# Optimization experiments

Measured on AMD Instinct MI355X. Metric: run time of the kernel, lower is better.

## Reference

```python
import jax, jax.numpy as jnp
import numpy as np

N = 1_000_000
_I = np.arange(12)[:, None]
IDX1 = (2 * _I + np.array([-1, 0, 1])) % 24        # [12,3] neighbor gather for net1
IDX2 = (2 * _I + np.array([0, 1, 2])) % 24         # [12,3] for net2
IDX3 = (2 * _I + np.array([0, 1, 2, 3])) % 24      # [12,4] for net3
IDX_U1 = np.array([i for i in range(36) if i % 3 != 2])  # 24 columns kept
IDX_A = np.arange(-1, 33, 3) % 36                  # u[:, -1::3] style gather (12,)
IDX_B = np.arange(2, 36, 3)                        # (12,)


def _mlp(x, w0, b0, w1, b1, w2, b2):
    h = jax.nn.relu(x @ w0.T + b0)
    h = jax.nn.relu(h @ w1.T + b1)
    return h @ w2.T + b2


def setup_inputs() -> dict:
    key = jax.random.key(0)
    ks = jax.random.split(key, 24)
    d = {
        "t": 0,
        "u": jax.random.normal(ks[0], (N, 36), dtype=jnp.float32),
        "reg": jax.random.normal(ks[1], (37,), dtype=jnp.float32),
    }
    shapes = {
        "n1_w0": (3, 3), "n1_b0": (3,), "n1_w1": (6, 3), "n1_b1": (6,), "n1_w2": (3, 6), "n1_b2": (3,),
        "n2_w0": (3, 3), "n2_b0": (3,), "n2_w1": (6, 3), "n2_b1": (6,), "n2_w2": (3, 6), "n2_b2": (3,),
        "n3_w0": (4, 4), "n3_b0": (4,), "n3_w1": (6, 4), "n3_b1": (6,), "n3_w2": (2, 6), "n3_b2": (2,),
    }
    for i, (name, shp) in enumerate(shapes.items()):
        d[name] = jax.random.normal(ks[2 + i], shp, dtype=jnp.float32) * 0.3
    return d


def reference(t, u, reg,
              n1_w0, n1_b0, n1_w1, n1_b1, n1_w2, n1_b2,
              n2_w0, n2_b0, n2_w1, n2_b1, n2_w2, n2_b2,
              n3_w0, n3_b0, n3_w1, n3_b1, n3_w2, n3_b2):
    outreg = u * reg[1:] + reg[0]                 # [N,36]
    u1 = u[:, IDX_U1]                              # [N,24]
    x1 = u1[:, IDX1]                               # [N,12,3]
    x2 = u1[:, IDX2]                               # [N,12,3]
    x3 = u1[:, IDX3]                               # [N,12,4]
    o1 = _mlp(x1, n1_w0, n1_b0, n1_w1, n1_b1, n1_w2, n1_b2)  # [N,12,3]
    o2 = _mlp(x2, n2_w0, n2_b0, n2_w1, n2_b1, n2_w2, n2_b2)  # [N,12,3]
    o3 = _mlp(x3, n3_w0, n3_b0, n3_w1, n3_b1, n3_w2, n3_b2)  # [N,12,2]
    ua = u[:, IDX_A]                               # [N,12]
    ub = u[:, IDX_B]                               # [N,12]
    c0 = outreg[:, ::3] + o1[..., 0] + o1[..., 1] * ua + o1[..., 2] * ub
    c1 = outreg[:, 1::3] + o2[..., 0] + o2[..., 1] * ua + o2[..., 2] * ub
    c2 = outreg[:, 2::3] + o3[..., 0] + o3[..., 1] * ub
    # interleave back into strided slices ::3, 1::3, 2::3
    return jnp.stack([c0, c1, c2], axis=-1).reshape(u.shape[0], 36)
```

## Files before the change

### kernel.cpp

```cpp
#include <hip/hip_runtime.h>


typedef float f2 __attribute__((ext_vector_type(2)));

__device__ __forceinline__ f2 splat2(float x) { f2 v; v.x = x; v.y = x; return v; }
__device__ __forceinline__ f2 mk2(float a, float b) { f2 v; v.x = a; v.y = b; return v; }
__device__ __forceinline__ f2 fma2(f2 a, f2 b, f2 c) { return __builtin_elementwise_fma(a, b, c); }
__device__ __forceinline__ f2 relu2(f2 a) { return __builtin_elementwise_max(a, splat2(0.0f)); }

__device__ __forceinline__ void mlp_a2(f2 x0, f2 x1, f2 x2,
                                       const float* __restrict__ w0, const float* __restrict__ b0,
                                       const float* __restrict__ w1, const float* __restrict__ b1,
                                       const float* __restrict__ w2, const float* __restrict__ b2,
                                       f2& o0, f2& o1, f2& o2)
{
    f2 h0[3];
#pragma unroll
    for (int q = 0; q < 3; ++q) {
        f2 a = fma2(x0, splat2(w0[q*3+0]), splat2(b0[q]));
        a = fma2(x1, splat2(w0[q*3+1]), a);
        a = fma2(x2, splat2(w0[q*3+2]), a);
        h0[q] = relu2(a);
    }
    f2 h1[6];
#pragma unroll
    for (int q = 0; q < 6; ++q) {
        f2 a = fma2(h0[0], splat2(w1[q*3+0]), splat2(b1[q]));
        a = fma2(h0[1], splat2(w1[q*3+1]), a);
        a = fma2(h0[2], splat2(w1[q*3+2]), a);
        h1[q] = relu2(a);
    }
    f2 t[3];
#pragma unroll
    for (int q = 0; q < 3; ++q) {
        f2 a = fma2(h1[0], splat2(w2[q*6+0]), splat2(b2[q]));
#pragma unroll
        for (int i = 1; i < 6; ++i) a = fma2(h1[i], splat2(w2[q*6+i]), a);
        t[q] = a;
    }
    o0 = t[0]; o1 = t[1]; o2 = t[2];
}

__device__ __forceinline__ void mlp_b2(f2 x0, f2 x1, f2 x2, f2 x3,
                                       const float* __restrict__ w0, const float* __restrict__ b0,
                                       const float* __restrict__ w1, const float* __restrict__ b1,
                                       const float* __restrict__ w2, const float* __restrict__ b2,
                                       f2& o0, f2& o1)
{
    f2 h0[4];
#pragma unroll
    for (int q = 0; q < 4; ++q) {
        f2 a = fma2(x0, splat2(w0[q*4+0]), splat2(b0[q]));
        a = fma2(x1, splat2(w0[q*4+1]), a);
        a = fma2(x2, splat2(w0[q*4+2]), a);
        a = fma2(x3, splat2(w0[q*4+3]), a);
        h0[q] = relu2(a);
    }
    f2 h1[6];
#pragma unroll
    for (int q = 0; q < 6; ++q) {
        f2 a = fma2(h0[0], splat2(w1[q*4+0]), splat2(b1[q]));
        a = fma2(h0[1], splat2(w1[q*4+1]), a);
        a = fma2(h0[2], splat2(w1[q*4+2]), a);
        a = fma2(h0[3], splat2(w1[q*4+3]), a);
        h1[q] = relu2(a);
    }
    f2 t[2];
#pragma unroll
    for (int q = 0; q < 2; ++q) {
        f2 a = fma2(h1[0], splat2(w2[q*6+0]), splat2(b2[q]));
#pragma unroll
        for (int i = 1; i < 6; ++i) a = fma2(h1[i], splat2(w2[q*6+i]), a);
        t[q] = a;
    }
    o0 = t[0]; o1 = t[1];
}

#define ROWS_PB 64
#define TPB 192

__global__ __launch_bounds__(TPB) void mixmodel_kernel(
    const float* __restrict__ u, const float* __restrict__ reg,
    const float* __restrict__ w10, const float* __restrict__ b10,
    const float* __restrict__ w11, const float* __restrict__ b11,
    const float* __restrict__ w12, const float* __restrict__ b12,
    const float* __restrict__ w20, const float* __restrict__ b20,
    const float* __restrict__ w21, const float* __restrict__ b21,
    const float* __restrict__ w22, const float* __restrict__ b22,
    const float* __restrict__ w30, const float* __restrict__ b30,
    const float* __restrict__ w31, const float* __restrict__ b31,
    const float* __restrict__ w32, const float* __restrict__ b32,
    float* __restrict__ out, int n)
{
    __shared__ float4 s4[ROWS_PB * 9];
    __shared__ float  sreg[37];

    const int brow = blockIdx.x * ROWS_PB;

    {
        const float4* __restrict__ g = reinterpret_cast<const float4*>(u + (size_t)brow * 36);
        const int wid  = threadIdx.x >> 6;
        const int lane = threadIdx.x & 63;
#pragma unroll
        for (int w = 0; w < 3; ++w) {
            const int base = w * TPB + wid * 64;
            __builtin_amdgcn_global_load_lds(
                (const __attribute__((address_space(1))) void*)(g + base + lane),
                (__attribute__((address_space(3))) void*)(s4 + base),
                16, 0, 0);
        }
    }
    if (threadIdx.x < 37) sreg[threadIdx.x] = reg[threadIdx.x];
    asm volatile("s_waitcnt vmcnt(0)" ::: "memory");
    __syncthreads();

    const int rl = threadIdx.x / 3;
    const int r  = threadIdx.x - 3 * rl;
    const int row = brow + rl;
    if (row >= n) return;

    float w_[20];
#pragma unroll
    for (int t = 0; t < 5; ++t) {
        int idx = 3 * r + 8 + t;
        if (idx >= 9) idx -= 9;
        if (idx >= 9) idx -= 9;
        const float4 v = s4[rl * 9 + idx];
        w_[4*t+0] = v.x; w_[4*t+1] = v.y; w_[4*t+2] = v.z; w_[4*t+3] = v.w;
    }
#define W(k) w_[(k) + 4]

    const f2 r02 = splat2(sreg[0]);
    const float* rb = sreg + 12 * r;

    f2 c0[2], c1[2], c2[2];

#pragma unroll
    for (int P = 0; P < 2; ++P) {
        const int q = 6 * P;
        f2 a0, a1, a2;
        mlp_a2(mk2(W(q - 2), W(q + 1)), mk2(W(q), W(q + 3)), mk2(W(q + 1), W(q + 4)),
               w10, b10, w11, b11, w12, b12, a0, a1, a2);
        const f2 ua = mk2(W(q - 1), W(q + 2));
        const f2 ub = mk2(W(q + 2), W(q + 5));
        const f2 rv = mk2(rb[q + 1], rb[q + 4]);
        const f2 uv = mk2(W(q), W(q + 3));
        c0[P] = fma2(uv, rv, r02) + fma2(a2, ub, fma2(a1, ua, a0));
    }
#pragma unroll
    for (int P = 0; P < 2; ++P) {
        const int q = 6 * P;
        f2 a0, a1, a2;
        mlp_a2(mk2(W(q), W(q + 3)), mk2(W(q + 1), W(q + 4)), mk2(W(q + 3), W(q + 6)),
               w20, b20, w21, b21, w22, b22, a0, a1, a2);
        const f2 ua = mk2(W(q - 1), W(q + 2));
        const f2 ub = mk2(W(q + 2), W(q + 5));
        const f2 rv = mk2(rb[q + 2], rb[q + 5]);
        const f2 uv = mk2(W(q + 1), W(q + 4));
        c1[P] = fma2(uv, rv, r02) + fma2(a2, ub, fma2(a1, ua, a0));
    }
#pragma unroll
    for (int P = 0; P < 2; ++P) {
        const int q = 6 * P;
        f2 d0, d1;
        mlp_b2(mk2(W(q), W(q + 3)), mk2(W(q + 1), W(q + 4)),
               mk2(W(q + 3), W(q + 6)), mk2(W(q + 4), W(q + 7)),
               w30, b30, w31, b31, w32, b32, d0, d1);
        const f2 ub = mk2(W(q + 2), W(q + 5));
        const f2 rv = mk2(rb[q + 3], rb[q + 6]);
        c2[P] = fma2(ub, rv, r02) + fma2(d1, ub, d0);
    }
#undef W

    float4* __restrict__ o4 = reinterpret_cast<float4*>(out + (size_t)row * 36 + 12 * r);
    o4[0] = make_float4(c0[0].x, c1[0].x, c2[0].x, c0[0].y);
    o4[1] = make_float4(c1[0].y, c2[0].y, c0[1].x, c1[1].x);
    o4[2] = make_float4(c2[1].x, c0[1].y, c1[1].y, c2[1].y);
}

extern "C" void kernel_launch(void* const* d_in, const int* in_sizes, int n_in,
                              void* d_out, int out_size, void* d_ws, size_t ws_size,
                              hipStream_t stream)
{
    const float* u   = (const float*)d_in[1];
    const float* reg = (const float*)d_in[2];
    const float* w10 = (const float*)d_in[3];
    const float* b10 = (const float*)d_in[4];
    const float* w11 = (const float*)d_in[5];
    const float* b11 = (const float*)d_in[6];
    const float* w12 = (const float*)d_in[7];
    const float* b12 = (const float*)d_in[8];
    const float* w20 = (const float*)d_in[9];
    const float* b20 = (const float*)d_in[10];
    const float* w21 = (const float*)d_in[11];
    const float* b21 = (const float*)d_in[12];
    const float* w22 = (const float*)d_in[13];
    const float* b22 = (const float*)d_in[14];
    const float* w30 = (const float*)d_in[15];
    const float* b30 = (const float*)d_in[16];
    const float* w31 = (const float*)d_in[17];
    const float* b31 = (const float*)d_in[18];
    const float* w32 = (const float*)d_in[19];
    const float* b32 = (const float*)d_in[20];
    float* out = (float*)d_out;

    const int n = in_sizes[1] / 36;
    const int grid = (n + ROWS_PB - 1) / ROWS_PB;

    hipLaunchKernelGGL(mixmodel_kernel, dim3(grid), dim3(TPB), 0, stream,
                       u, reg, w10, b10, w11, b11, w12, b12,
                       w20, b20, w21, b21, w22, b22,
                       w30, b30, w31, b31, w32, b32, out, n);
}
```

Measured before the change: 71.05 us.

## Remap threads to row pairs with f2 packing across rows and nontemporal stores

```diff
diff --git a/kernel.cpp b/kernel.cpp
--- a/kernel.cpp
+++ b/kernel.cpp
@@ -114,68 +114,61 @@
     asm volatile("s_waitcnt vmcnt(0)" ::: "memory");
     __syncthreads();
 
-    const int rl = threadIdx.x / 3;
-    const int r  = threadIdx.x - 3 * rl;
-    const int row = brow + rl;
-    if (row >= n) return;
-
-    float w_[20];
-#pragma unroll
-    for (int t = 0; t < 5; ++t) {
-        int idx = 3 * r + 8 + t;
-        if (idx >= 9) idx -= 9;
-        if (idx >= 9) idx -= 9;
-        const float4 v = s4[rl * 9 + idx];
-        w_[4*t+0] = v.x; w_[4*t+1] = v.y; w_[4*t+2] = v.z; w_[4*t+3] = v.w;
-    }
-#define W(k) w_[(k) + 4]
+    const int t  = threadIdx.x;
+    const int rp = t / 6;
+    const int s  = t - 6 * rp;
+
+    const float* sf = reinterpret_cast<const float*>(s4);
+    const int va  = rp * 72 + 6 * s;
+    const int vaP = va - 2 + (s == 0 ? 36 : 0);
+    const int vaT = va + (s == 5 ? -36 : 0);
+
+    f2 P[10];
+#pragma unroll
+    for (int k = 0; k < 2; ++k) { P[k].x = sf[vaP + k];     P[k].y = sf[vaP + k + 36]; }
+#pragma unroll
+    for (int k = 0; k < 6; ++k) { P[k + 2].x = sf[va + k];  P[k + 2].y = sf[va + k + 36]; }
+#pragma unroll
+    for (int k = 6; k < 8; ++k) { P[k + 2].x = sf[vaT + k]; P[k + 2].y = sf[vaT + k + 36]; }
 
     const f2 r02 = splat2(sreg[0]);
-    const float* rb = sreg + 12 * r;
-
-    f2 c0[2], c1[2], c2[2];
-
-#pragma unroll
-    for (int P = 0; P < 2; ++P) {
-        const int q = 6 * P;
+    const float* rb = sreg + 6 * s;
+
+    f2 c_[6];
+
+#pragma unroll
+    for (int J = 0; J < 2; ++J) {
+        const int b = 3 * J;
         f2 a0, a1, a2;
-        mlp_a2(mk2(W(q - 2), W(q + 1)), mk2(W(q), W(q + 3)), mk2(W(q + 1), W(q + 4)),
-               w10, b10, w11, b11, w12, b12, a0, a1, a2);
-        const f2 ua = mk2(W(q - 1), W(q + 2));
-        const f2 ub = mk2(W(q + 2), W(q + 5));
-        const f2 rv = mk2(rb[q + 1], rb[q + 4]);
-        const f2 uv = mk2(W(q), W(q + 3));
-        c0[P] = fma2(uv, rv, r02) + fma2(a2, ub, fma2(a1, ua, a0));
-    }
-#pragma unroll
-    for (int P = 0; P < 2; ++P) {
-        const int q = 6 * P;
+        mlp_a2(P[b], P[b + 2], P[b + 3], w10, b10, w11, b11, w12, b12, a0, a1, a2);
+        c_[3*J + 0] = fma2(P[b + 2], splat2(rb[b + 1]), r02)
+                    + fma2(a2, P[b + 4], fma2(a1, P[b + 1], a0));
+    }
+#pragma unroll
+    for (int J = 0; J < 2; ++J) {
+        const int b = 3 * J;
         f2 a0, a1, a2;
-        mlp_a2(mk2(W(q), W(q + 3)), mk2(W(q + 1), W(q + 4)), mk2(W(q + 3), W(q + 6)),
-               w20, b20, w21, b21, w22, b22, a0, a1, a2);
-        const f2 ua = mk2(W(q - 1), W(q + 2));
-        const f2 ub = mk2(W(q + 2), W(q + 5));
-        const f2 rv = mk2(rb[q + 2], rb[q + 5]);
-        const f2 uv = mk2(W(q + 1), W(q + 4));
-        c1[P] = fma2(uv, rv, r02) + fma2(a2, ub, fma2(a1, ua, a0));
-    }
-#pragma unroll
-    for (int P = 0; P < 2; ++P) {
-        const int q = 6 * P;
+        mlp_a2(P[b + 2], P[b + 3], P[b + 5], w20, b20, w21, b21, w22, b22, a0, a1, a2);
+        c_[3*J + 1] = fma2(P[b + 3], splat2(rb[b + 2]), r02)
+                    + fma2(a2, P[b + 4], fma2(a1, P[b + 1], a0));
+    }
+#pragma unroll
+    for (int J = 0; J < 2; ++J) {
+        const int b = 3 * J;
         f2 d0, d1;
-        mlp_b2(mk2(W(q), W(q + 3)), mk2(W(q + 1), W(q + 4)),
-               mk2(W(q + 3), W(q + 6)), mk2(W(q + 4), W(q + 7)),
-               w30, b30, w31, b31, w32, b32, d0, d1);
-        const f2 ub = mk2(W(q + 2), W(q + 5));
-        const f2 rv = mk2(rb[q + 3], rb[q + 6]);
-        c2[P] = fma2(ub, rv, r02) + fma2(d1, ub, d0);
-    }
-#undef W
-
-    float4* __restrict__ o4 = reinterpret_cast<float4*>(out + (size_t)row * 36 + 12 * r);
-    o4[0] = make_float4(c0[0].x, c1[0].x, c2[0].x, c0[0].y);
-    o4[1] = make_float4(c1[0].y, c2[0].y, c0[1].x, c1[1].x);
-    o4[2] = make_float4(c2[1].x, c0[1].y, c1[1].y, c2[1].y);
+        mlp_b2(P[b + 2], P[b + 3], P[b + 5], P[b + 6], w30, b30, w31, b31, w32, b32, d0, d1);
+        c_[3*J + 2] = fma2(P[b + 4], splat2(rb[b + 3]), r02)
+                    + fma2(d1, P[b + 4], d0);
+    }
+
+    float* oA = out + (size_t)(brow + 2 * rp) * 36 + 6 * s;
+    float* oB = oA + 36;
+    __builtin_nontemporal_store(mk2(c_[0].x, c_[1].x), (f2*)(oA + 0));
+    __builtin_nontemporal_store(mk2(c_[2].x, c_[3].x), (f2*)(oA + 2));
+    __builtin_nontemporal_store(mk2(c_[4].x, c_[5].x), (f2*)(oA + 4));
+    __builtin_nontemporal_store(mk2(c_[0].y, c_[1].y), (f2*)(oB + 0));
+    __builtin_nontemporal_store(mk2(c_[2].y, c_[3].y), (f2*)(oB + 2));
+    __builtin_nontemporal_store(mk2(c_[4].y, c_[5].y), (f2*)(oB + 4));
 }
 
 extern "C" void kernel_launch(void* const* d_in, const int* in_sizes, int n_in,
```

Measured after the change: 65.18 us. -8.3%, faster.
